# Kernel tuning notes

Measured on AMD Instinct MI355X. Metric: run time of the kernel, lower is better.

Reference implementation:

```python
import jax, jax.numpy as jnp
import numpy as np

N, E, R, T = 50000, 800000, 3, 16
IV, IS, IP, H, C = 64, 64, 32, 128, 2
# d=2 filter coefficients (ascending powers of x), order: lf, bernstein(3), hf
THETAS = [
    [0.8, -0.5],            # lf: (0.3 + 1/2 - x/2)
    [3.0, -3.0, 0.75],      # bernstein i=0
    [0.0, 3.0, -1.5],       # bernstein i=1
    [0.0, 0.0, 0.75],       # bernstein i=2
    [-0.2, 0.5],            # hf: (0.3 - 1/2 + x/2)
]


def setup_inputs() -> dict:
    key = jax.random.key(0)
    ks = iter(jax.random.split(key, 64))
    rn = lambda *s: jax.random.normal(next(ks), s, jnp.float32)
    w = lambda *s: rn(*s) * 0.05
    inp = {
        'voc_features': rn(N, T, IV),
        'sms_features': rn(N, T, IS),
        'personal_feature': rn(N, IP),
        # LSTM params (torch gate order i,f,g,o)
        'Wih_v': w(4 * IV, IV), 'Whh_v': w(4 * IV, IV), 'bih_v': w(4 * IV), 'bhh_v': w(4 * IV),
        'Wih_s': w(4 * IS, IS), 'Whh_s': w(4 * IS, IS), 'bih_s': w(4 * IS), 'bhh_s': w(4 * IS),
        'W_lin': w(H, IV), 'b_lin': w(H),
        'W_lin1': w(H, IS), 'b_lin1': w(H),
        'W_pers': w(H, IP), 'b_pers': w(H),
        'W_lin2': w(H, 2 * H), 'b_lin2': w(H),
        'W_lin3': w(H, 2 * H), 'b_lin3': w(H),
        'W_lin4': w(H, 4 * H), 'b_lin4': w(H),
        'W_lin5': w(R, H, H), 'b_lin5': w(R, H),
        'Wf1': w(R, H, H), 'bf1': w(R, H), 'Wf2': w(R, H),
        'W_lin6': w(C, 6 * H), 'b_lin6': w(C),
        'src': jax.random.randint(next(ks), (R, E), 0, N, jnp.int32),
        'dst': jax.random.randint(next(ks), (R, E), 0, N, jnp.int32),
    }
    return inp


def _lstm_last(x, Wih, Whh, bih, bhh):
    n, _, _ = x.shape
    h_dim = Whh.shape[1]
    b = bih + bhh

    def step(carry, xt):
        h, c = carry
        g = xt @ Wih.T + h @ Whh.T + b
        i, f, gg, o = jnp.split(g, 4, axis=-1)
        c = jax.nn.sigmoid(f) * c + jax.nn.sigmoid(i) * jnp.tanh(gg)
        h = jax.nn.sigmoid(o) * jnp.tanh(c)
        return (h, c), None

    init = (jnp.zeros((n, h_dim), x.dtype), jnp.zeros((n, h_dim), x.dtype))
    (h, _), _ = jax.lax.scan(step, init, jnp.swapaxes(x, 0, 1))
    return h  # last hidden state == output at last timestep


def _polyconv(theta, feat, s, d, dinv):
    h = theta[0] * feat
    f = feat
    for k in range(1, len(theta)):
        m = f * dinv
        agg = jax.ops.segment_sum(m[s], d, num_segments=N)  # copy_u + sum
        f = f - agg * dinv
        h = h + theta[k] * f
    return h


def reference(voc_features, sms_features, personal_feature,
              Wih_v, Whh_v, bih_v, bhh_v, Wih_s, Whh_s, bih_s, bhh_s,
              W_lin, b_lin, W_lin1, b_lin1, W_pers, b_pers,
              W_lin2, b_lin2, W_lin3, b_lin3, W_lin4, b_lin4,
              W_lin5, b_lin5, Wf1, bf1, Wf2, W_lin6, b_lin6, src, dst):
    act = lambda x: jax.nn.leaky_relu(x, 0.01)
    xv = _lstm_last(voc_features, Wih_v, Whh_v, bih_v, bhh_v) @ W_lin.T + b_lin
    xs = _lstm_last(sms_features, Wih_s, Whh_s, bih_s, bhh_s) @ W_lin1.T + b_lin1
    xp = personal_feature @ W_pers.T + b_pers
    xv = act(jnp.concatenate([xv, xp], axis=1))  # [N, 2H]
    xs = act(jnp.concatenate([xs, xp], axis=1))
    xvs = jnp.concatenate([xv, xs], axis=1)      # [N, 4H]
    x_in = [act(xv @ W_lin2.T + b_lin2),
            act(xs @ W_lin3.T + b_lin3),
            act(xvs @ W_lin4.T + b_lin4)]        # each [N, H]

    h_all = []
    for r in range(R):
        s, d = src[r], dst[r]
        deg = jax.ops.segment_sum(jnp.ones((E,), jnp.float32), d, num_segments=N)
        dinv = jnp.clip(deg, 1.0, None) ** -0.5
        dinv = dinv[:, None]
        h_filters = jnp.stack([_polyconv(th, x_in[r], s, d, dinv) for th in THETAS], axis=1)  # [N, 5, H]
        score = jnp.einsum('nfh,h->nf', jnp.tanh(jnp.einsum('nfh,oh->nfo', h_filters, Wf1[r]) + bf1[r]), Wf2[r])
        soft = jax.nn.softmax(score, axis=1)[:, :, None]
        res = (soft * h_filters).sum(1)          # [N, H]
        h_all.append(res @ W_lin5[r].T + b_lin5[r])

    h = act(jnp.concatenate(h_all, axis=1))      # [N, 3H]
    h = jnp.concatenate([h, x_in[0], x_in[1], x_in[2]], axis=1)  # [N, 6H]
    return h @ W_lin6.T + b_lin6
```

## Files before the change

kernel.cpp:

```cpp
#include <hip/hip_runtime.h>
#include <math.h>

#define NN 50000
#define EE 800000
#define RR 3
#define CHUNK 10000

__device__ __forceinline__ float leaky(float x){ return x > 0.f ? x : 0.01f*x; }
__device__ __forceinline__ float sigmoid_f(float x){ return 1.f/(1.f+__expf(-x)); }
__device__ __forceinline__ float tanh_f(float x){ return 1.f - 2.f/(__expf(2.f*x)+1.f); }

#define GT_BM 64
#define GT_BN 128
#define GT_BK 32
#define GT_PA 68
#define GT_PW 132

__global__ __launch_bounds__(256) void gemm_tiled(
    const float* __restrict__ A, int M, int lda, int koff, int K,
    const float* __restrict__ W,
    const float* __restrict__ bias, const float* __restrict__ bias2,
    float* __restrict__ D, int ldd, int doff,
    float* __restrict__ D2, int doff2, int act)
{
  __shared__ float As[GT_BK * GT_PA];
  __shared__ float Ws[GT_BK * GT_PW];

  const int tid   = threadIdx.x;
  const int bm    = blockIdx.x * GT_BM;
  const int wrow0 = blockIdx.y * GT_BN;
  const int tx = tid & 15;
  const int ty = tid >> 4;
  const int m0 = ty * 4;
  const int n0 = tx * 4;

  const int srow = tid >> 3;
  const int skq  = tid & 7;

  float acc[4][8];
#pragma unroll
  for (int i=0;i<4;i++)
#pragma unroll
    for (int j=0;j<8;j++) acc[i][j]=0.f;

  float4 ra[2], rw[4];
  auto load_tiles = [&](int kc){
#pragma unroll
    for (int p=0;p<2;p++){
      int gr = bm + p*32 + srow; if (gr >= M) gr = M-1;
      ra[p] = *(const float4*)(A + (size_t)gr*lda + koff + kc + skq*4);
    }
#pragma unroll
    for (int p=0;p<4;p++){
      int r = p*32 + srow;
      rw[p] = *(const float4*)(W + (size_t)(wrow0 + r)*K + kc + skq*4);
    }
  };

  load_tiles(0);
  for (int kc = 0; kc < K; kc += GT_BK){
    if (kc) __syncthreads();
#pragma unroll
    for (int p=0;p<2;p++){
      int r = p*32 + srow;
      As[(skq*4+0)*GT_PA + r] = ra[p].x;
      As[(skq*4+1)*GT_PA + r] = ra[p].y;
      As[(skq*4+2)*GT_PA + r] = ra[p].z;
      As[(skq*4+3)*GT_PA + r] = ra[p].w;
    }
#pragma unroll
    for (int p=0;p<4;p++){
      int r = p*32 + srow;
      Ws[(skq*4+0)*GT_PW + r] = rw[p].x;
      Ws[(skq*4+1)*GT_PW + r] = rw[p].y;
      Ws[(skq*4+2)*GT_PW + r] = rw[p].z;
      Ws[(skq*4+3)*GT_PW + r] = rw[p].w;
    }
    __syncthreads();
    if (kc + GT_BK < K) load_tiles(kc + GT_BK);

#pragma unroll
    for (int k = 0; k < GT_BK; ++k){
      const float4 av = *(const float4*)&As[k*GT_PA + m0];
      const float4 w0 = *(const float4*)&Ws[k*GT_PW + n0];
      const float4 w1 = *(const float4*)&Ws[k*GT_PW + n0 + 64];
      const float am[4] = {av.x, av.y, av.z, av.w};
#pragma unroll
      for (int i=0;i<4;i++){
        acc[i][0] = fmaf(am[i], w0.x, acc[i][0]);
        acc[i][1] = fmaf(am[i], w0.y, acc[i][1]);
        acc[i][2] = fmaf(am[i], w0.z, acc[i][2]);
        acc[i][3] = fmaf(am[i], w0.w, acc[i][3]);
        acc[i][4] = fmaf(am[i], w1.x, acc[i][4]);
        acc[i][5] = fmaf(am[i], w1.y, acc[i][5]);
        acc[i][6] = fmaf(am[i], w1.z, acc[i][6]);
        acc[i][7] = fmaf(am[i], w1.w, acc[i][7]);
      }
    }
  }

  float4 bA = *(const float4*)(bias + wrow0 + n0);
  float4 bB = *(const float4*)(bias + wrow0 + n0 + 64);
  if (bias2){
    const float4 cA = *(const float4*)(bias2 + wrow0 + n0);
    const float4 cB = *(const float4*)(bias2 + wrow0 + n0 + 64);
    bA.x+=cA.x; bA.y+=cA.y; bA.z+=cA.z; bA.w+=cA.w;
    bB.x+=cB.x; bB.y+=cB.y; bB.z+=cB.z; bB.w+=cB.w;
  }

#pragma unroll
  for (int i=0;i<4;i++){
    const int r = bm + m0 + i;
    if (r >= M) continue;
    float4 v0 = {acc[i][0]+bA.x, acc[i][1]+bA.y, acc[i][2]+bA.z, acc[i][3]+bA.w};
    float4 v1 = {acc[i][4]+bB.x, acc[i][5]+bB.y, acc[i][6]+bB.z, acc[i][7]+bB.w};
    if (act){
      v0.x=leaky(v0.x); v0.y=leaky(v0.y); v0.z=leaky(v0.z); v0.w=leaky(v0.w);
      v1.x=leaky(v1.x); v1.y=leaky(v1.y); v1.z=leaky(v1.z); v1.w=leaky(v1.w);
    }
    *(float4*)(D + (size_t)r*ldd + doff + wrow0 + n0)      = v0;
    *(float4*)(D + (size_t)r*ldd + doff + wrow0 + n0 + 64) = v1;
    if (D2){
      *(float4*)(D2 + (size_t)r*ldd + doff2 + wrow0 + n0)      = v0;
      *(float4*)(D2 + (size_t)r*ldd + doff2 + wrow0 + n0 + 64) = v1;
    }
  }
}

__global__ __launch_bounds__(128, 2) void lstm_rec_kernel(
    const float* __restrict__ xg,
    const float* __restrict__ Whh,
    float* __restrict__ hout)
{
  const int t  = threadIdx.x;
  const int nb = blockIdx.x * 16;
  __shared__ float hs[16*64];
  __shared__ float cs[16*64];
  __shared__ float gs[16*256];

  const int j0 = t, j1 = t + 128;
  float4 wA[16], wB[16];
#pragma unroll
  for (int i=0;i<16;i++){
    wA[i] = *(const float4*)(Whh + (size_t)j0*64 + i*4);
    wB[i] = *(const float4*)(Whh + (size_t)j1*64 + i*4);
  }

  for (int i = t; i < 16*64; i += 128){ hs[i]=0.f; cs[i]=0.f; }
  __syncthreads();

  for (int step = 0; step < 16; ++step){
    float xgA[16], xgB[16];
#pragma unroll
    for (int n=0;n<16;n++){
      const size_t base = ((size_t)(nb+n)*16 + step)*256;
      xgA[n] = xg[base + j0];
      xgB[n] = xg[base + j1];
    }

#pragma unroll 4
    for (int n = 0; n < 16; ++n){
      float4 aA = {0.f,0.f,0.f,0.f};
      float4 aB = {0.f,0.f,0.f,0.f};
#pragma unroll
      for (int kc = 0; kc < 16; ++kc){
        const float4 hv = *(const float4*)&hs[n*64 + kc*4];
        aA.x = fmaf(wA[kc].x, hv.x, aA.x);
        aA.y = fmaf(wA[kc].y, hv.y, aA.y);
        aA.z = fmaf(wA[kc].z, hv.z, aA.z);
        aA.w = fmaf(wA[kc].w, hv.w, aA.w);
        aB.x = fmaf(wB[kc].x, hv.x, aB.x);
        aB.y = fmaf(wB[kc].y, hv.y, aB.y);
        aB.z = fmaf(wB[kc].z, hv.z, aB.z);
        aB.w = fmaf(wB[kc].w, hv.w, aB.w);
      }
      gs[n*256 + j0] = (aA.x + aA.y) + (aA.z + aA.w) + xgA[n];
      gs[n*256 + j1] = (aB.x + aB.y) + (aB.z + aB.w) + xgB[n];
    }
    __syncthreads();
#pragma unroll
    for (int p = 0; p < 8; ++p){
      const int idx = p*128 + t;
      const int n = idx >> 6, k = idx & 63;
      const float gi = gs[n*256 + k];
      const float gf = gs[n*256 + 64 + k];
      const float gg = gs[n*256 + 128 + k];
      const float go = gs[n*256 + 192 + k];
      float c = sigmoid_f(gf)*cs[idx] + sigmoid_f(gi)*tanh_f(gg);
      cs[idx] = c; hs[idx] = sigmoid_f(go)*tanh_f(c);
    }
    __syncthreads();
  }
#pragma unroll
  for (int p = 0; p < 2; ++p){
    const int q = p*128 + t;
    const int ln = q >> 4, lk = (q & 15)*4;
    *(float4*)(hout + (size_t)(nb+ln)*64 + lk) = *(float4*)&hs[ln*64 + lk];
  }
}

__global__ void hist_kernel(const int* __restrict__ dst, int* __restrict__ cnt){
  const int r = blockIdx.y;
  const int e = blockIdx.x*256 + threadIdx.x;
  if (e < EE) atomicAdd(&cnt[(size_t)r*NN + dst[(size_t)r*EE + e]], 1);
}

__global__ void dinv_kernel(const int* __restrict__ cnt, float* __restrict__ dinv){
  int i = blockIdx.x*256 + threadIdx.x;
  if (i < RR*NN) dinv[i] = 1.f/sqrtf(fmaxf((float)cnt[i], 1.f));
}

__global__ __launch_bounds__(256) void scan_kernel(
    const int* __restrict__ cnt, int* __restrict__ row_ptr)
{
  const int r = blockIdx.x;
  const int tid = threadIdx.x;
  const int* c = cnt + (size_t)r*NN;
  int* rp = row_ptr + (size_t)r*(NN+1);
  __shared__ int sdata[256];
  int running = 0;
  for (int chunk = 0; chunk < NN; chunk += 1024){
    __syncthreads();
    int idx = chunk + tid*4;
    int v0=0,v1=0,v2=0,v3=0;
    if (idx   < NN) v0 = c[idx];
    if (idx+1 < NN) v1 = c[idx+1];
    if (idx+2 < NN) v2 = c[idx+2];
    if (idx+3 < NN) v3 = c[idx+3];
    int s = v0+v1+v2+v3;
    sdata[tid] = s;
    __syncthreads();
    for (int off=1; off<256; off<<=1){
      int t = (tid >= off) ? sdata[tid-off] : 0;
      __syncthreads();
      sdata[tid] += t;
      __syncthreads();
    }
    int excl = running + sdata[tid] - s;
    if (idx   < NN) rp[idx]   = excl;
    if (idx+1 < NN) rp[idx+1] = excl + v0;
    if (idx+2 < NN) rp[idx+2] = excl + v0 + v1;
    if (idx+3 < NN) rp[idx+3] = excl + v0 + v1 + v2;
    running += sdata[255];
  }
  if (tid == 0) rp[NN] = running;
}

__global__ void fill_kernel(const int* __restrict__ src, const int* __restrict__ dst,
                            const int* __restrict__ row_ptr, int* __restrict__ cursor,
                            int* __restrict__ csr_src)
{
  const int r = blockIdx.y;
  const int e = blockIdx.x*256 + threadIdx.x;
  if (e >= EE) return;
  const int d = dst[(size_t)r*EE + e];
  const int pos = atomicAdd(&cursor[(size_t)r*NN + d], 1);
  csr_src[(size_t)r*EE + row_ptr[(size_t)r*(NN+1) + d] + pos] = src[(size_t)r*EE + e];
}

__global__ __launch_bounds__(256) void gather_fused(
    const int* __restrict__ csr_src, const int* __restrict__ row_ptr,
    const float* __restrict__ f, const float* __restrict__ dinv,
    float* __restrict__ fn)
{
  const int node = blockIdx.x*4 + (threadIdx.x >> 6);
  const int lane = threadIdx.x & 63;
  if (node >= NN) return;
  int p  = row_ptr[node];
  const int p1 = row_ptr[node+1];
  float a0 = 0.f, a1 = 0.f;
  for (; p + 2 <= p1; p += 2){
    const int s0 = csr_src[p];
    const int s1 = csr_src[p+1];
    const float d0 = dinv[s0];
    const float d1 = dinv[s1];
    const float f00 = f[(size_t)s0*128 + lane];
    const float f01 = f[(size_t)s0*128 + 64 + lane];
    const float f10 = f[(size_t)s1*128 + lane];
    const float f11 = f[(size_t)s1*128 + 64 + lane];
    a0 = fmaf(f00, d0, a0); a1 = fmaf(f01, d0, a1);
    a0 = fmaf(f10, d1, a0); a1 = fmaf(f11, d1, a1);
  }
  if (p < p1){
    const int s0 = csr_src[p];
    const float d0 = dinv[s0];
    a0 = fmaf(f[(size_t)s0*128 + lane], d0, a0);
    a1 = fmaf(f[(size_t)s0*128 + 64 + lane], d0, a1);
  }
  const float dvd = dinv[node];
  fn[(size_t)node*128 + lane]      = f[(size_t)node*128 + lane]      - a0*dvd;
  fn[(size_t)node*128 + 64 + lane] = f[(size_t)node*128 + 64 + lane] - a1*dvd;
}

__global__ __launch_bounds__(128) void combine_kernel(
    const float* __restrict__ f0, const float* __restrict__ f1, const float* __restrict__ f2,
    const float* __restrict__ Wf1, const float* __restrict__ bf1, const float* __restrict__ Wf2,
    const float* __restrict__ W5, const float* __restrict__ b5,
    float* __restrict__ hall, int rcol)
{
  const int o = threadIdx.x;
  const int nb = blockIdx.x * 8;
  __shared__ float fs[3*8*128];
  __shared__ float red[16];

  for (int i = o; i < 768; i += 128){
    int e = i*4;
    int jj = e >> 10; int rem = e & 1023;
    int n = rem >> 7; int k = rem & 127;
    const float* fp = (jj==0) ? f0 : ((jj==1) ? f1 : f2);
    *(float4*)&fs[e] = *(const float4*)(fp + (size_t)(nb+n)*128 + k);
  }
  __syncthreads();

  float u0[8],u1[8],u2[8],w0[8],w1[8],w2[8];
#pragma unroll
  for (int n=0;n<8;n++){u0[n]=0;u1[n]=0;u2[n]=0;w0[n]=0;w1[n]=0;w2[n]=0;}

  for (int kc=0;kc<32;kc++){
    const float4 wa = *(const float4*)(Wf1 + (size_t)o*128 + kc*4);
    const float4 wb = *(const float4*)(W5  + (size_t)o*128 + kc*4);
#pragma unroll
    for (int n=0;n<8;n++){
      const float4 a0 = *(const float4*)&fs[0*1024 + n*128 + kc*4];
      const float4 a1 = *(const float4*)&fs[1*1024 + n*128 + kc*4];
      const float4 a2 = *(const float4*)&fs[2*1024 + n*128 + kc*4];
      u0[n] = fmaf(wa.x,a0.x, fmaf(wa.y,a0.y, fmaf(wa.z,a0.z, fmaf(wa.w,a0.w, u0[n]))));
      u1[n] = fmaf(wa.x,a1.x, fmaf(wa.y,a1.y, fmaf(wa.z,a1.z, fmaf(wa.w,a1.w, u1[n]))));
      u2[n] = fmaf(wa.x,a2.x, fmaf(wa.y,a2.y, fmaf(wa.z,a2.z, fmaf(wa.w,a2.w, u2[n]))));
      w0[n] = fmaf(wb.x,a0.x, fmaf(wb.y,a0.y, fmaf(wb.z,a0.z, fmaf(wb.w,a0.w, w0[n]))));
      w1[n] = fmaf(wb.x,a1.x, fmaf(wb.y,a1.y, fmaf(wb.z,a1.z, fmaf(wb.w,a1.w, w1[n]))));
      w2[n] = fmaf(wb.x,a2.x, fmaf(wb.y,a2.y, fmaf(wb.z,a2.z, fmaf(wb.w,a2.w, w2[n]))));
    }
  }

  const float bo = bf1[o], wf2o = Wf2[o], b5o = b5[o];
#pragma unroll
  for (int n=0;n<8;n++){
    float s0 = wf2o * tanh_f(fmaf( 0.8f,u0[n], fmaf(-0.5f,u1[n], bo)));
    float s1 = wf2o * tanh_f(fmaf( 3.0f,u0[n], fmaf(-3.0f,u1[n], fmaf(0.75f,u2[n], bo))));
    float s2 = wf2o * tanh_f(fmaf( 3.0f,u1[n], fmaf(-1.5f,u2[n], bo)));
    float s3 = wf2o * tanh_f(fmaf(0.75f,u2[n], bo));
    float s4 = wf2o * tanh_f(fmaf(-0.2f,u0[n], fmaf( 0.5f,u1[n], bo)));
#pragma unroll
    for (int off=32; off>0; off>>=1){
      s0 += __shfl_xor(s0, off);
      s1 += __shfl_xor(s1, off);
      s2 += __shfl_xor(s2, off);
      s3 += __shfl_xor(s3, off);
      s4 += __shfl_xor(s4, off);
    }
    if ((o & 63) == 0){
      const int w = o >> 6;
      red[w*8+0]=s0; red[w*8+1]=s1; red[w*8+2]=s2; red[w*8+3]=s3; red[w*8+4]=s4;
    }
    __syncthreads();
    float t0 = red[0]+red[8], t1 = red[1]+red[9], t2 = red[2]+red[10],
          t3 = red[3]+red[11], t4 = red[4]+red[12];
    float mx = fmaxf(fmaxf(fmaxf(t0,t1),fmaxf(t2,t3)),t4);
    float e0=__expf(t0-mx), e1=__expf(t1-mx), e2=__expf(t2-mx),
          e3=__expf(t3-mx), e4=__expf(t4-mx);
    float inv = 1.f/(e0+e1+e2+e3+e4);
    e0*=inv; e1*=inv; e2*=inv; e3*=inv; e4*=inv;
    float c0 =  0.8f*e0 + 3.0f*e1              - 0.2f*e4;
    float c1 = -0.5f*e0 - 3.0f*e1 + 3.0f*e2    + 0.5f*e4;
    float c2 =            0.75f*e1 - 1.5f*e2 + 0.75f*e3;
    float outv = fmaf(c0,w0[n], fmaf(c1,w1[n], fmaf(c2,w2[n], b5o)));
    hall[(size_t)(nb+n)*384 + rcol + o] = outv;
    __syncthreads();
  }
}

__global__ __launch_bounds__(256) void final_kernel(
    const float* __restrict__ hall, const float* __restrict__ xin,
    const float* __restrict__ W6, const float* __restrict__ b6,
    float* __restrict__ out)
{
  const int n = blockIdx.x*256 + threadIdx.x;
  if (n >= NN) return;
  float a0 = b6[0], a1 = b6[1];
  const float* h = hall + (size_t)n*384;
#pragma unroll 8
  for (int jc=0;jc<96;jc++){
    float4 v = *(const float4*)(h + jc*4);
    v.x = leaky(v.x); v.y = leaky(v.y); v.z = leaky(v.z); v.w = leaky(v.w);
    const float4 wA = *(const float4*)(W6 + jc*4);
    const float4 wB = *(const float4*)(W6 + 768 + jc*4);
    a0 = fmaf(wA.x,v.x, fmaf(wA.y,v.y, fmaf(wA.z,v.z, fmaf(wA.w,v.w, a0))));
    a1 = fmaf(wB.x,v.x, fmaf(wB.y,v.y, fmaf(wB.z,v.z, fmaf(wB.w,v.w, a1))));
  }
  for (int p=0;p<3;p++){
    const float* xp = xin + (size_t)p*NN*128 + (size_t)n*128;
    const int jb = 384 + p*128;
#pragma unroll 8
    for (int jc=0;jc<32;jc++){
      const float4 v = *(const float4*)(xp + jc*4);
      const float4 wA = *(const float4*)(W6 + jb + jc*4);
      const float4 wB = *(const float4*)(W6 + 768 + jb + jc*4);
      a0 = fmaf(wA.x,v.x, fmaf(wA.y,v.y, fmaf(wA.z,v.z, fmaf(wA.w,v.w, a0))));
      a1 = fmaf(wB.x,v.x, fmaf(wB.y,v.y, fmaf(wB.z,v.z, fmaf(wB.w,v.w, a1))));
    }
  }
  out[(size_t)n*2+0] = a0;
  out[(size_t)n*2+1] = a1;
}

extern "C" void kernel_launch(void* const* d_in, const int* in_sizes, int n_in,
                              void* d_out, int out_size, void* d_ws, size_t ws_size,
                              hipStream_t stream)
{
  (void)in_sizes; (void)n_in; (void)out_size; (void)ws_size;
  const float* voc    = (const float*)d_in[0];
  const float* sms    = (const float*)d_in[1];
  const float* pers   = (const float*)d_in[2];
  const float* Wih_v  = (const float*)d_in[3];
  const float* Whh_v  = (const float*)d_in[4];
  const float* bih_v  = (const float*)d_in[5];
  const float* bhh_v  = (const float*)d_in[6];
  const float* Wih_s  = (const float*)d_in[7];
  const float* Whh_s  = (const float*)d_in[8];
  const float* bih_s  = (const float*)d_in[9];
  const float* bhh_s  = (const float*)d_in[10];
  const float* W_lin  = (const float*)d_in[11];
  const float* b_lin  = (const float*)d_in[12];
  const float* W_lin1 = (const float*)d_in[13];
  const float* b_lin1 = (const float*)d_in[14];
  const float* W_pers = (const float*)d_in[15];
  const float* b_pers = (const float*)d_in[16];
  const float* W_lin2 = (const float*)d_in[17];
  const float* b_lin2 = (const float*)d_in[18];
  const float* W_lin3 = (const float*)d_in[19];
  const float* b_lin3 = (const float*)d_in[20];
  const float* W_lin4 = (const float*)d_in[21];
  const float* b_lin4 = (const float*)d_in[22];
  const float* W_lin5 = (const float*)d_in[23];
  const float* b_lin5 = (const float*)d_in[24];
  const float* Wf1    = (const float*)d_in[25];
  const float* bf1    = (const float*)d_in[26];
  const float* Wf2    = (const float*)d_in[27];
  const float* W_lin6 = (const float*)d_in[28];
  const float* b_lin6 = (const float*)d_in[29];
  const int*   src    = (const int*)d_in[30];
  const int*   dst    = (const int*)d_in[31];

  float* ws   = (float*)d_ws;
  float* hv   = ws;
  float* hs   = hv  + (size_t)NN*64;
  float* cat  = hs  + (size_t)NN*64;
  float* xin  = cat + (size_t)NN*512;
  float* f1   = xin + (size_t)3*NN*128;
  float* f2   = f1  + (size_t)NN*128;
  float* dinv = f2  + (size_t)NN*128;
  int*   cnt     = (int*)(dinv + (size_t)RR*NN);
  int*   row_ptr = cnt + (size_t)RR*NN;
  int*   cursor  = row_ptr + (size_t)RR*(NN+1);
  int*   csr_src = cursor + (size_t)RR*NN;
  float* hall = cat;
  float* xg   = cat;
  float* out  = (float*)d_out;

  for (int ls = 0; ls < 2; ++ls){
    const float* xi  = ls ? sms   : voc;
    const float* Wih = ls ? Wih_s : Wih_v;
    const float* Whh = ls ? Whh_s : Whh_v;
    const float* bi  = ls ? bih_s : bih_v;
    const float* bh  = ls ? bhh_s : bhh_v;
    float* ho        = ls ? hs    : hv;
    for (int n0 = 0; n0 < NN; n0 += CHUNK){
      dim3 gx((CHUNK*16)/GT_BM, 2);
      gemm_tiled<<<gx, 256, 0, stream>>>(
          xi + (size_t)n0*16*64, CHUNK*16, 64, 0, 64,
          Wih, bi, bh, xg, 256, 0, nullptr, 0, 0);
      lstm_rec_kernel<<<CHUNK/16, 128, 0, stream>>>(
          xg, Whh, ho + (size_t)n0*64);
    }
  }

  hipMemsetAsync(cnt, 0, (size_t)RR*NN*sizeof(int), stream);
  hipMemsetAsync(cursor, 0, (size_t)RR*NN*sizeof(int), stream);
  hist_kernel<<<dim3(EE/256, RR), 256, 0, stream>>>(dst, cnt);
  dinv_kernel<<<(RR*NN+255)/256, 256, 0, stream>>>(cnt, dinv);
  scan_kernel<<<RR, 256, 0, stream>>>(cnt, row_ptr);
  fill_kernel<<<dim3(EE/256, RR), 256, 0, stream>>>(src, dst, row_ptr, cursor, csr_src);

  const int gB = (NN + GT_BM - 1) / GT_BM;

  gemm_tiled<<<dim3(gB,1), 256, 0, stream>>>(hv,   NN, 64, 0, 64, W_lin,  b_lin,  nullptr, cat, 512,   0, nullptr, 0, 1);
  gemm_tiled<<<dim3(gB,1), 256, 0, stream>>>(hs,   NN, 64, 0, 64, W_lin1, b_lin1, nullptr, cat, 512, 256, nullptr, 0, 1);
  gemm_tiled<<<dim3(gB,1), 256, 0, stream>>>(pers, NN, 32, 0, 32, W_pers, b_pers, nullptr, cat, 512, 128, cat, 384, 1);

  gemm_tiled<<<dim3(gB,1), 256, 0, stream>>>(cat, NN, 512,   0, 256, W_lin2, b_lin2, nullptr, xin,                    128, 0, nullptr, 0, 1);
  gemm_tiled<<<dim3(gB,1), 256, 0, stream>>>(cat, NN, 512, 256, 256, W_lin3, b_lin3, nullptr, xin + (size_t)NN*128,   128, 0, nullptr, 0, 1);
  gemm_tiled<<<dim3(gB,1), 256, 0, stream>>>(cat, NN, 512,   0, 512, W_lin4, b_lin4, nullptr, xin + (size_t)2*NN*128, 128, 0, nullptr, 0, 1);

  for (int r = 0; r < RR; ++r){
    const float* f0 = xin + (size_t)r*NN*128;
    const float* dv = dinv + (size_t)r*NN;
    const int* cs = csr_src + (size_t)r*EE;
    const int* rp = row_ptr + (size_t)r*(NN+1);

    gather_fused<<<(NN+3)/4, 256, 0, stream>>>(cs, rp, f0, dv, f1);
    gather_fused<<<(NN+3)/4, 256, 0, stream>>>(cs, rp, f1, dv, f2);

    combine_kernel<<<NN/8, 128, 0, stream>>>(f0, f1, f2,
        Wf1 + (size_t)r*128*128, bf1 + (size_t)r*128, Wf2 + (size_t)r*128,
        W_lin5 + (size_t)r*128*128, b_lin5 + (size_t)r*128, hall, r*128);
  }

  final_kernel<<<(NN+255)/256, 256, 0, stream>>>(hall, xin, W_lin6, b_lin6, out);
}
```

Measured before the change: 4.471 ms.

## Fuse LSTM input projection into the recurrent kernel, dropping the xg buffer

```diff
diff --git a/kernel.cpp b/kernel.cpp
--- a/kernel.cpp
+++ b/kernel.cpp
@@ -4,7 +4,6 @@
 #define NN 50000
 #define EE 800000
 #define RR 3
-#define CHUNK 10000
 
 __device__ __forceinline__ float leaky(float x){ return x > 0.f ? x : 0.01f*x; }
 __device__ __forceinline__ float sigmoid_f(float x){ return 1.f/(1.f+__expf(-x)); }
@@ -127,60 +126,63 @@
   }
 }
 
-__global__ __launch_bounds__(128, 2) void lstm_rec_kernel(
-    const float* __restrict__ xg,
+__global__ __launch_bounds__(256, 2) void lstm_fused(
+    const float* __restrict__ x,
+    const float* __restrict__ Wih,
     const float* __restrict__ Whh,
+    const float* __restrict__ bih, const float* __restrict__ bhh,
     float* __restrict__ hout)
 {
-  const int t  = threadIdx.x;
+  const int j  = threadIdx.x;
   const int nb = blockIdx.x * 16;
+  __shared__ float xs[16*64];
   __shared__ float hs[16*64];
   __shared__ float cs[16*64];
   __shared__ float gs[16*256];
 
-  const int j0 = t, j1 = t + 128;
-  float4 wA[16], wB[16];
+  float4 wi[16], wh[16];
 #pragma unroll
   for (int i=0;i<16;i++){
-    wA[i] = *(const float4*)(Whh + (size_t)j0*64 + i*4);
-    wB[i] = *(const float4*)(Whh + (size_t)j1*64 + i*4);
-  }
-
-  for (int i = t; i < 16*64; i += 128){ hs[i]=0.f; cs[i]=0.f; }
-  __syncthreads();
-
-  for (int step = 0; step < 16; ++step){
-    float xgA[16], xgB[16];
-#pragma unroll
-    for (int n=0;n<16;n++){
-      const size_t base = ((size_t)(nb+n)*16 + step)*256;
-      xgA[n] = xg[base + j0];
-      xgB[n] = xg[base + j1];
-    }
+    wi[i] = *(const float4*)(Wih + (size_t)j*64 + i*4);
+    wh[i] = *(const float4*)(Whh + (size_t)j*64 + i*4);
+  }
+  const float bj = bih[j] + bhh[j];
+
+  for (int i = j; i < 16*64; i += 256){ hs[i]=0.f; cs[i]=0.f; }
+
+  const int sn = j >> 4;
+  const int sk = (j & 15) * 4;
+
+  for (int t = 0; t < 16; ++t){
+    *(float4*)&xs[sn*64 + sk] =
+        *(const float4*)(x + ((size_t)(nb+sn)*16 + t)*64 + sk);
+    __syncthreads();
 
 #pragma unroll 4
     for (int n = 0; n < 16; ++n){
-      float4 aA = {0.f,0.f,0.f,0.f};
-      float4 aB = {0.f,0.f,0.f,0.f};
+      float4 ax = {0.f,0.f,0.f,0.f};
+      float4 ah = {0.f,0.f,0.f,0.f};
 #pragma unroll
       for (int kc = 0; kc < 16; ++kc){
+        const float4 xv = *(const float4*)&xs[n*64 + kc*4];
         const float4 hv = *(const float4*)&hs[n*64 + kc*4];
-        aA.x = fmaf(wA[kc].x, hv.x, aA.x);
-        aA.y = fmaf(wA[kc].y, hv.y, aA.y);
-        aA.z = fmaf(wA[kc].z, hv.z, aA.z);
-        aA.w = fmaf(wA[kc].w, hv.w, aA.w);
-        aB.x = fmaf(wB[kc].x, hv.x, aB.x);
-        aB.y = fmaf(wB[kc].y, hv.y, aB.y);
-        aB.z = fmaf(wB[kc].z, hv.z, aB.z);
-        aB.w = fmaf(wB[kc].w, hv.w, aB.w);
+        ax.x = fmaf(wi[kc].x, xv.x, ax.x);
+        ax.y = fmaf(wi[kc].y, xv.y, ax.y);
+        ax.z = fmaf(wi[kc].z, xv.z, ax.z);
+        ax.w = fmaf(wi[kc].w, xv.w, ax.w);
+        ah.x = fmaf(wh[kc].x, hv.x, ah.x);
+        ah.y = fmaf(wh[kc].y, hv.y, ah.y);
+        ah.z = fmaf(wh[kc].z, hv.z, ah.z);
+        ah.w = fmaf(wh[kc].w, hv.w, ah.w);
       }
-      gs[n*256 + j0] = (aA.x + aA.y) + (aA.z + aA.w) + xgA[n];
-      gs[n*256 + j1] = (aB.x + aB.y) + (aB.z + aB.w) + xgB[n];
-    }
-    __syncthreads();
-#pragma unroll
-    for (int p = 0; p < 8; ++p){
-      const int idx = p*128 + t;
+      gs[n*256 + j] = ((ax.x + ax.y) + (ax.z + ax.w))
+                    + ((ah.x + ah.y) + (ah.z + ah.w)) + bj;
+    }
+    __syncthreads();
+
+#pragma unroll
+    for (int p = 0; p < 4; ++p){
+      const int idx = p*256 + j;
       const int n = idx >> 6, k = idx & 63;
       const float gi = gs[n*256 + k];
       const float gf = gs[n*256 + 64 + k];
@@ -189,14 +191,10 @@
       float c = sigmoid_f(gf)*cs[idx] + sigmoid_f(gi)*tanh_f(gg);
       cs[idx] = c; hs[idx] = sigmoid_f(go)*tanh_f(c);
     }
-    __syncthreads();
-  }
-#pragma unroll
-  for (int p = 0; p < 2; ++p){
-    const int q = p*128 + t;
-    const int ln = q >> 4, lk = (q & 15)*4;
-    *(float4*)(hout + (size_t)(nb+ln)*64 + lk) = *(float4*)&hs[ln*64 + lk];
-  }
+  }
+  __syncthreads();
+  const int ln = j >> 4, lk = (j & 15)*4;
+  *(float4*)(hout + (size_t)(nb+ln)*64 + lk) = *(float4*)&hs[ln*64 + lk];
 }
 
 __global__ void hist_kernel(const int* __restrict__ dst, int* __restrict__ cnt){
@@ -455,25 +453,10 @@
   int*   cursor  = row_ptr + (size_t)RR*(NN+1);
   int*   csr_src = cursor + (size_t)RR*NN;
   float* hall = cat;
-  float* xg   = cat;
   float* out  = (float*)d_out;
 
-  for (int ls = 0; ls < 2; ++ls){
-    const float* xi  = ls ? sms   : voc;
-    const float* Wih = ls ? Wih_s : Wih_v;
-    const float* Whh = ls ? Whh_s : Whh_v;
-    const float* bi  = ls ? bih_s : bih_v;
-    const float* bh  = ls ? bhh_s : bhh_v;
-    float* ho        = ls ? hs    : hv;
-    for (int n0 = 0; n0 < NN; n0 += CHUNK){
-      dim3 gx((CHUNK*16)/GT_BM, 2);
-      gemm_tiled<<<gx, 256, 0, stream>>>(
-          xi + (size_t)n0*16*64, CHUNK*16, 64, 0, 64,
-          Wih, bi, bh, xg, 256, 0, nullptr, 0, 0);
-      lstm_rec_kernel<<<CHUNK/16, 128, 0, stream>>>(
-          xg, Whh, ho + (size_t)n0*64);
-    }
-  }
+  lstm_fused<<<NN/16, 256, 0, stream>>>(voc, Wih_v, Whh_v, bih_v, bhh_v, hv);
+  lstm_fused<<<NN/16, 256, 0, stream>>>(sms, Wih_s, Whh_s, bih_s, bhh_s, hs);
 
   hipMemsetAsync(cnt, 0, (size_t)RR*NN*sizeof(int), stream);
   hipMemsetAsync(cursor, 0, (size_t)RR*NN*sizeof(int), stream);
```

Measured after the change: 14.59 ms. +226.3%, slower.
